# Optimization experiments

Hardware: AMD Instinct MI355X
Metric: run time of the kernel (lower is better)

## Reference

```python
import jax, jax.numpy as jnp
import numpy as np

DIM_MODEL = 512
INV_SCALE = DIM_MODEL ** (-0.5)  # NOTE: source DIVIDES by this, i.e. multiplies scores by sqrt(d)


def setup_inputs() -> dict:
    key = jax.random.key(0)
    ks = jax.random.split(key, 9)
    B, LQ, LKV, D = 32, 64, 4096, DIM_MODEL
    lim = 1.0 / np.sqrt(D)  # torch Linear default init range
    return {
        "x1": jax.random.normal(ks[0], (B, LQ, D), dtype=jnp.float32),
        "x2": jax.random.normal(ks[1], (B, LKV, D), dtype=jnp.float32),
        "mask": jnp.zeros((B, LQ, LKV), dtype=bool),
        "wq": jax.random.uniform(ks[2], (D, D), jnp.float32, -lim, lim),
        "bq": jax.random.uniform(ks[3], (D,), jnp.float32, -lim, lim),
        "wk": jax.random.uniform(ks[4], (D, D), jnp.float32, -lim, lim),
        "bk": jax.random.uniform(ks[5], (D,), jnp.float32, -lim, lim),
        "wv": jax.random.uniform(ks[6], (D, D), jnp.float32, -lim, lim),
        "bv": jax.random.uniform(ks[7], (D,), jnp.float32, -lim, lim),
    }


def reference(x1, x2, mask, wq, bq, wk, bk, wv, bv):
    # torch.nn.Linear: y = x @ W^T + b
    q = jnp.einsum("bqd,ed->bqe", x1, wq) + bq          # [B, LQ, D]
    k = jnp.einsum("bkd,ed->bke", x2, wk) + bk          # [B, LKV, D]
    v = jnp.einsum("bkd,ed->bke", x2, wv) + bv          # [B, LKV, D]
    qk = jnp.einsum("bqd,bkd->bqk", q, k)               # [B, LQ, LKV]
    scaled_qk = qk / INV_SCALE                           # faithful: divide by d^-0.5
    p = jax.nn.softmax(scaled_qk, axis=-1)
    # dropout p=0.0 -> identity; mask is unused in the original forward
    return jnp.einsum("bqk,bkd->bqd", p, v)              # [B, LQ, D]
```

## Files before the change

### kernel.cpp

```cpp
#include <hip/hip_runtime.h>
#include <math.h>


#define LQ 64
#define LKV 4096
#define NB 32
#define DM 512
#define SCALE 22.627416997969522f
#define KEYS_TOTAL (NB * LKV)
#define NCHUNK 16
#define CHUNK 256
#define PBS 264

typedef __attribute__((ext_vector_type(8))) short bf16x8;
typedef __attribute__((ext_vector_type(4))) float f32x4;
typedef __attribute__((ext_vector_type(8))) unsigned short u16x8;
typedef __attribute__((ext_vector_type(4))) unsigned short u16x4;

__device__ __forceinline__ unsigned short f2bf(float f) {
    unsigned u = __float_as_uint(f);
    u += 0x7fffu + ((u >> 16) & 1u);
    return (unsigned short)(u >> 16);
}
__device__ __forceinline__ float bf2f(unsigned short s) {
    return __uint_as_float(((unsigned)s) << 16);
}
__device__ __forceinline__ void gld16(const void* g, void* l) {
    __builtin_amdgcn_global_load_lds(
        (const __attribute__((address_space(1))) unsigned int*)g,
        (__attribute__((address_space(3))) unsigned int*)l, 16, 0, 0);
}

__device__ __forceinline__ void split8_body(const float* __restrict__ src,
                                            unsigned short* __restrict__ hi,
                                            unsigned short* __restrict__ lo, int blk) {
    size_t idx = ((size_t)blk * 256 + threadIdx.x) * 8;
    float4 a = *(const float4*)(src + idx);
    float4 b = *(const float4*)(src + idx + 4);
    float ff[8] = {a.x, a.y, a.z, a.w, b.x, b.y, b.z, b.w};
    u16x8 h, l;
#pragma unroll
    for (int i = 0; i < 8; ++i) {
        h[i] = f2bf(ff[i]);
        l[i] = f2bf(ff[i] - bf2f(h[i]));
    }
    *(u16x8*)(hi + idx) = h;
    *(u16x8*)(lo + idx) = l;
}

__global__ __launch_bounds__(256) void prep_kernel(
        const float* __restrict__ x1, const float* __restrict__ wq,
        const float* __restrict__ wk, const float* __restrict__ wv,
        unsigned short* __restrict__ x1h, unsigned short* __restrict__ x1l,
        unsigned short* __restrict__ wqh, unsigned short* __restrict__ wql,
        unsigned short* __restrict__ wkth, unsigned short* __restrict__ wktl,
        unsigned short* __restrict__ wvh, unsigned short* __restrict__ wvl) {
    __shared__ float T[64 * 65];
    int bid = blockIdx.x;
    if (bid < 512) { split8_body(x1, x1h, x1l, bid); return; }
    bid -= 512;
    if (bid < 128) { split8_body(wq, wqh, wql, bid); return; }
    bid -= 128;
    if (bid < 64) {
        const int bx = (bid & 7) * 64, by = (bid >> 3) * 64;
        const int t = threadIdx.x, col = t & 63, rg = t >> 6;
#pragma unroll
        for (int i = 0; i < 16; ++i) {
            int row = i * 4 + rg;
            T[col * 65 + row] = wk[(size_t)(by + row) * DM + bx + col];
        }
        __syncthreads();
#pragma unroll
        for (int i = 0; i < 16; ++i) {
            int row = i * 4 + rg;
            float v = T[row * 65 + col];
            unsigned short h = f2bf(v);
            wkth[(size_t)(bx + row) * DM + by + col] = h;
            wktl[(size_t)(bx + row) * DM + by + col] = f2bf(v - bf2f(h));
        }
        return;
    }
    bid -= 64;
    split8_body(wv, wvh, wvl, bid);
}

__global__ __launch_bounds__(256) void sgemm_kernel(
        const unsigned short* __restrict__ Ah_g, const unsigned short* __restrict__ Al_g,
        const unsigned short* __restrict__ Bh_g, const unsigned short* __restrict__ Bl_g,
        const float* __restrict__ bias, int mode,
        unsigned short* __restrict__ out0, unsigned short* __restrict__ out2l,
        float* __restrict__ outf) {
    __shared__ unsigned short smem[16384];
    unsigned short* Ah = smem;
    unsigned short* Al = smem + 4096;
    unsigned short* Bh = smem + 8192;
    unsigned short* Bl = smem + 12288;

    const int bn = blockIdx.x, bm = blockIdx.y;
    const int t = threadIdx.x, w = t >> 6, l = t & 63;
    const int wm = (w >> 1) * 64, wn = (w & 1) * 64;
    const int c16 = l & 15, q = l >> 4, q8 = q << 3;
    const int rB = l >> 2, cB = (l & 3) << 3;

    f32x4 acc[4][4];
#pragma unroll
    for (int i = 0; i < 4; ++i)
#pragma unroll
        for (int jj = 0; jj < 4; ++jj) acc[i][jj] = (f32x4){0.f,0.f,0.f,0.f};

    for (int k0 = 0; k0 < DM; k0 += 32) {
#pragma unroll
        for (int jj = 0; jj < 2; ++jj) {
            int r = w * 32 + jj * 16;
            size_t ga = (size_t)(bm * 128 + r + rB) * DM + k0 + cB;
            gld16(Ah_g + ga, &Ah[r * 32]);
            gld16(Al_g + ga, &Al[r * 32]);
            size_t gb = (size_t)(bn * 128 + r + rB) * DM + k0 + cB;
            gld16(Bh_g + gb, &Bh[r * 32]);
            gld16(Bl_g + gb, &Bl[r * 32]);
        }
        __syncthreads();
        bf16x8 ah[4], al[4];
#pragma unroll
        for (int mt = 0; mt < 4; ++mt) {
            ah[mt] = *(const bf16x8*)&Ah[(wm + mt*16 + c16) * 32 + q8];
            al[mt] = *(const bf16x8*)&Al[(wm + mt*16 + c16) * 32 + q8];
        }
#pragma unroll
        for (int nt = 0; nt < 4; ++nt) {
            bf16x8 bh = *(const bf16x8*)&Bh[(wn + nt*16 + c16) * 32 + q8];
            bf16x8 bl = *(const bf16x8*)&Bl[(wn + nt*16 + c16) * 32 + q8];
#pragma unroll
            for (int mt = 0; mt < 4; ++mt) {
                acc[mt][nt] = __builtin_amdgcn_mfma_f32_16x16x32_bf16(ah[mt], bh, acc[mt][nt], 0, 0, 0);
                acc[mt][nt] = __builtin_amdgcn_mfma_f32_16x16x32_bf16(al[mt], bh, acc[mt][nt], 0, 0, 0);
                acc[mt][nt] = __builtin_amdgcn_mfma_f32_16x16x32_bf16(ah[mt], bl, acc[mt][nt], 0, 0, 0);
            }
        }
        __syncthreads();
    }

#pragma unroll
    for (int mt = 0; mt < 4; ++mt)
#pragma unroll
        for (int nt = 0; nt < 4; ++nt) {
            int col = bn * 128 + wn + nt * 16 + c16;
            float bia = bias ? bias[col] : 0.f;
#pragma unroll
            for (int r = 0; r < 4; ++r) {
                size_t row = (size_t)bm * 128 + wm + mt * 16 + q * 4 + r;
                float y = acc[mt][nt][r] + bia;
                if (mode == 0) {
                    unsigned short h = f2bf(y);
                    out0[row * 1024 + col]       = h;
                    out0[row * 1024 + 512 + col] = f2bf(y - bf2f(h));
                } else if (mode == 1) {
                    outf[row * 512 + col] = y;
                } else {
                    unsigned short h = f2bf(y);
                    out0[row * 512 + col]  = h;
                    out2l[row * 512 + col] = f2bf(y - bf2f(h));
                }
            }
        }
}

__global__ __launch_bounds__(256) void prepVt_kernel(const float* __restrict__ src,
        unsigned short* __restrict__ x2ht) {
    __shared__ unsigned short T[128 * 136];
    const int d0 = blockIdx.x * 128, k0 = blockIdx.y * 128;
    const int t = threadIdx.x;
    const int cg = t & 31, rg = t >> 5;
#pragma unroll
    for (int i = 0; i < 16; ++i) {
        int row = i * 8 + rg;
        float4 v = *(const float4*)(src + (size_t)(k0 + row) * DM + d0 + cg * 4);
        float ff[4] = {v.x, v.y, v.z, v.w};
        int rsw = row ^ ((cg & 15) << 3);
#pragma unroll
        for (int j = 0; j < 4; ++j)
            T[(cg * 4 + j) * 136 + rsw] = f2bf(ff[j]);
    }
    __syncthreads();
#pragma unroll
    for (int ii = 0; ii < 8; ++ii) {
        int dl = ii * 16 + (t >> 4);
        int ko = (t & 15) * 8;
        u16x8 vv = *(const u16x8*)&T[dl * 136 + (ko ^ (((dl >> 2) & 15) << 3))];
        *(u16x8*)(x2ht + (size_t)(d0 + dl) * KEYS_TOTAL + k0 + ko) = vv;
    }
}

__global__ __launch_bounds__(512, 4) void attn_kernel(
        const unsigned short* __restrict__ Q2,
        const float* __restrict__ x2f,
        const unsigned short* __restrict__ Vt,
        float* __restrict__ Opart,
        float* __restrict__ ML) {
    __shared__ char smem_raw[81920];
    unsigned short* Pb = (unsigned short*)smem_raw;
    float* redb = (float*)(smem_raw + 66560);
    float* mrow = (float*)(smem_raw + 68608);
    float* lrow = (float*)(smem_raw + 68864);

    const int c = blockIdx.x, b = blockIdx.y;
    const int t = threadIdx.x, w = t >> 6, l = t & 63;
    const int c16 = l & 15, q = l >> 4, q8 = q << 3;
    const int rB = l >> 2, cB = (l & 3) << 3;
    const int rF = l >> 3, cF = (l & 7) << 2;
    const size_t key0 = (size_t)b * LKV + (size_t)c * CHUNK;

    f32x4 acc[4][2];
#pragma unroll
    for (int i = 0; i < 4; ++i)
#pragma unroll
        for (int jj = 0; jj < 2; ++jj) acc[i][jj] = (f32x4){0.f,0.f,0.f,0.f};

    auto stageQK = [&](int s, int k0) {
        char* base = smem_raw + s * 40960;
        unsigned short* Qh = (unsigned short*)base;
        unsigned short* Ql = (unsigned short*)(base + 4096);
        float* Kf = (float*)(base + 8192);
        if (w < 4)
            gld16(Q2 + (size_t)(b * 64 + w * 16 + rB) * 1024 + k0 + cB, &Qh[(w * 16) * 32]);
        else
            gld16(Q2 + (size_t)(b * 64 + (w - 4) * 16 + rB) * 1024 + 512 + k0 + cB, &Ql[((w - 4) * 16) * 32]);
#pragma unroll
        for (int i = 0; i < 4; ++i) {
            int r = w * 32 + i * 8;
            gld16(x2f + (key0 + r + rF) * DM + k0 + cF, &Kf[r * 32]);
        }
    };

    stageQK(0, 0);
    __syncthreads();
#pragma unroll 1
    for (int k0 = 0; k0 < DM; k0 += 32) {
        const int s = (k0 >> 5) & 1;
        if (k0 + 32 < DM) stageQK(s ^ 1, k0 + 32);
        const unsigned short* Qh = (const unsigned short*)(smem_raw + s * 40960);
        const unsigned short* Ql = Qh + 2048;
        const float* Kf = (const float*)(smem_raw + s * 40960 + 8192);
        bf16x8 ah[4], al[4];
#pragma unroll
        for (int mt = 0; mt < 4; ++mt) {
            ah[mt] = *(const bf16x8*)&Qh[(mt * 16 + c16) * 32 + q8];
            al[mt] = *(const bf16x8*)&Ql[(mt * 16 + c16) * 32 + q8];
        }
#pragma unroll
        for (int nt = 0; nt < 2; ++nt) {
            const float* kp = &Kf[(w * 32 + nt * 16 + c16) * 32 + q8];
            float4 f0 = *(const float4*)kp;
            float4 f1 = *(const float4*)(kp + 4);
            float ff[8] = {f0.x, f0.y, f0.z, f0.w, f1.x, f1.y, f1.z, f1.w};
            bf16x8 bh, bl;
#pragma unroll
            for (int i2 = 0; i2 < 8; ++i2) {
                unsigned short hb = f2bf(ff[i2]);
                bh[i2] = (short)hb;
                bl[i2] = (short)f2bf(ff[i2] - bf2f(hb));
            }
#pragma unroll
            for (int mt = 0; mt < 4; ++mt) {
                acc[mt][nt] = __builtin_amdgcn_mfma_f32_16x16x32_bf16(ah[mt], bh, acc[mt][nt], 0, 0, 0);
                acc[mt][nt] = __builtin_amdgcn_mfma_f32_16x16x32_bf16(al[mt], bh, acc[mt][nt], 0, 0, 0);
                acc[mt][nt] = __builtin_amdgcn_mfma_f32_16x16x32_bf16(ah[mt], bl, acc[mt][nt], 0, 0, 0);
            }
        }
        __syncthreads();
    }

    auto stagePV = [&](int s, int h, int ks) {
        unsigned short* Vb = (unsigned short*)(smem_raw + 33792 + s * 16384);
#pragma unroll
        for (int jj = 0; jj < 2; ++jj) {
            int dloc = w * 32 + jj * 16;
            gld16(Vt + (size_t)(h * 256 + dloc + rB) * KEYS_TOTAL + key0 + ks * 32 + cB,
                  &Vb[dloc * 32]);
        }
    };
    stagePV(0, 0, 0);

#pragma unroll
    for (int mt = 0; mt < 4; ++mt)
#pragma unroll
        for (int nt = 0; nt < 2; ++nt)
#pragma unroll
            for (int r = 0; r < 4; ++r) acc[mt][nt][r] *= SCALE;

    float rmax_[4][4];
#pragma unroll
    for (int mt = 0; mt < 4; ++mt)
#pragma unroll
        for (int r = 0; r < 4; ++r)
            rmax_[mt][r] = fmaxf(acc[mt][0][r], acc[mt][1][r]);
#pragma unroll
    for (int off = 1; off < 16; off <<= 1)
#pragma unroll
        for (int mt = 0; mt < 4; ++mt)
#pragma unroll
            for (int r = 0; r < 4; ++r)
                rmax_[mt][r] = fmaxf(rmax_[mt][r], __shfl_xor(rmax_[mt][r], off));
    if (c16 == 0) {
#pragma unroll
        for (int mt = 0; mt < 4; ++mt)
#pragma unroll
            for (int r = 0; r < 4; ++r) redb[w * 64 + mt * 16 + q * 4 + r] = rmax_[mt][r];
    }
    __syncthreads();
    if (t < 64) {
        float m = redb[t];
#pragma unroll
        for (int ww = 1; ww < 8; ++ww) m = fmaxf(m, redb[ww * 64 + t]);
        mrow[t] = m;
    }
    __syncthreads();

    float rsum_[4][4];
#pragma unroll
    for (int mt = 0; mt < 4; ++mt)
#pragma unroll
        for (int r = 0; r < 4; ++r) {
            float m = mrow[mt * 16 + q * 4 + r];
            float s = 0.f;
#pragma unroll
            for (int nt = 0; nt < 2; ++nt) {
                float e = __expf(acc[mt][nt][r] - m);
                acc[mt][nt][r] = e;
                s += e;
            }
            rsum_[mt][r] = s;
        }
#pragma unroll
    for (int off = 1; off < 16; off <<= 1)
#pragma unroll
        for (int mt = 0; mt < 4; ++mt)
#pragma unroll
            for (int r = 0; r < 4; ++r) rsum_[mt][r] += __shfl_xor(rsum_[mt][r], off);
    if (c16 == 0) {
#pragma unroll
        for (int mt = 0; mt < 4; ++mt)
#pragma unroll
            for (int r = 0; r < 4; ++r) redb[w * 64 + mt * 16 + q * 4 + r] = rsum_[mt][r];
    }
    __syncthreads();
    if (t < 64) {
        float s = redb[t];
#pragma unroll
        for (int ww = 1; ww < 8; ++ww) s += redb[ww * 64 + t];
        lrow[t] = s;
    }
#pragma unroll
    for (int mt = 0; mt < 4; ++mt)
#pragma unroll
        for (int nt = 0; nt < 2; ++nt)
#pragma unroll
            for (int r = 0; r < 4; ++r)
                Pb[(mt * 16 + q * 4 + r) * PBS + w * 32 + nt * 16 + c16] = f2bf(acc[mt][nt][r]);
    __syncthreads();

    f32x4 accO[4][4];
#pragma unroll
    for (int i = 0; i < 4; ++i)
#pragma unroll
        for (int jj = 0; jj < 4; ++jj) accO[i][jj] = (f32x4){0.f,0.f,0.f,0.f};

#pragma unroll 1
    for (int ks = 0; ks < 8; ++ks) {
        const int s = ks & 1;
        if (ks < 7) stagePV(s ^ 1, 0, ks + 1);
        else        stagePV(s ^ 1, 1, 0);
        const unsigned short* Vb = (const unsigned short*)(smem_raw + 33792 + s * 16384);
        bf16x8 ap[4];
#pragma unroll
        for (int mt = 0; mt < 4; ++mt)
            ap[mt] = *(const bf16x8*)&Pb[(mt * 16 + c16) * PBS + ks * 32 + q8];
#pragma unroll
        for (int nt = 0; nt < 2; ++nt) {
            bf16x8 bvv = *(const bf16x8*)&Vb[(w * 32 + nt * 16 + c16) * 32 + q8];
#pragma unroll
            for (int mt = 0; mt < 4; ++mt)
                accO[mt][nt] = __builtin_amdgcn_mfma_f32_16x16x32_bf16(ap[mt], bvv, accO[mt][nt], 0, 0, 0);
        }
        __syncthreads();
    }
#pragma unroll 1
    for (int ks = 0; ks < 8; ++ks) {
        const int s = ks & 1;
        if (ks < 7) stagePV(s ^ 1, 1, ks + 1);
        const unsigned short* Vb = (const unsigned short*)(smem_raw + 33792 + s * 16384);
        bf16x8 ap[4];
#pragma unroll
        for (int mt = 0; mt < 4; ++mt)
            ap[mt] = *(const bf16x8*)&Pb[(mt * 16 + c16) * PBS + ks * 32 + q8];
#pragma unroll
        for (int nt = 0; nt < 2; ++nt) {
            bf16x8 bvv = *(const bf16x8*)&Vb[(w * 32 + nt * 16 + c16) * 32 + q8];
#pragma unroll
            for (int mt = 0; mt < 4; ++mt)
                accO[mt][2 + nt] = __builtin_amdgcn_mfma_f32_16x16x32_bf16(ap[mt], bvv, accO[mt][2 + nt], 0, 0, 0);
        }
        __syncthreads();
    }

    const size_t part = (size_t)b * NCHUNK + c;
#pragma unroll
    for (int mt = 0; mt < 4; ++mt)
#pragma unroll
        for (int h = 0; h < 2; ++h)
#pragma unroll
            for (int nt = 0; nt < 2; ++nt) {
                int col = h * 256 + w * 32 + nt * 16 + c16;
#pragma unroll
                for (int r = 0; r < 4; ++r)
                    Opart[(part * 64 + mt * 16 + q * 4 + r) * 512 + col] = accO[mt][h * 2 + nt][r];
            }
    if (t < 64) {
        ML[part * 128 + t]      = mrow[t];
        ML[part * 128 + 64 + t] = lrow[t];
    }
}

__global__ __launch_bounds__(128) void combine_kernel(const float* __restrict__ Opart,
                                                      const float* __restrict__ ML,
                                                      unsigned short* __restrict__ Uh,
                                                      unsigned short* __restrict__ Ul) {
    const int b = blockIdx.x >> 6, row = blockIdx.x & 63;
    const int t = threadIdx.x;
    float m[NCHUNK], lv[NCHUNK];
    float M = -1e30f;
#pragma unroll
    for (int c = 0; c < NCHUNK; ++c) {
        m[c]  = ML[(size_t)(b * NCHUNK + c) * 128 + row];
        lv[c] = ML[(size_t)(b * NCHUNK + c) * 128 + 64 + row];
        M = fmaxf(M, m[c]);
    }
    float den = 0.f, wgt[NCHUNK];
#pragma unroll
    for (int c = 0; c < NCHUNK; ++c) { wgt[c] = __expf(m[c] - M); den += wgt[c] * lv[c]; }
    float4 o = make_float4(0.f, 0.f, 0.f, 0.f);
#pragma unroll
    for (int c = 0; c < NCHUNK; ++c) {
        float4 v = *(const float4*)&Opart[((size_t)(b * NCHUNK + c) * 64 + row) * 512 + t * 4];
        o.x += wgt[c] * v.x; o.y += wgt[c] * v.y; o.z += wgt[c] * v.z; o.w += wgt[c] * v.w;
    }
    const float inv = 1.f / den;
    float rr[4] = {o.x * inv, o.y * inv, o.z * inv, o.w * inv};
    u16x4 h, lo_;
#pragma unroll
    for (int j = 0; j < 4; ++j) {
        h[j]   = f2bf(rr[j]);
        lo_[j] = f2bf(rr[j] - bf2f(h[j]));
    }
    size_t base = ((size_t)(b * 64 + row)) * 512 + t * 4;
    *(u16x4*)&Uh[base] = h;
    *(u16x4*)&Ul[base] = lo_;
}

extern "C" void kernel_launch(void* const* d_in, const int* in_sizes, int n_in,
                              void* d_out, int out_size, void* d_ws, size_t ws_size,
                              hipStream_t stream) {
    const float* x1 = (const float*)d_in[0];
    const float* x2 = (const float*)d_in[1];
    const float* wq = (const float*)d_in[3];
    const float* bq = (const float*)d_in[4];
    const float* wk = (const float*)d_in[5];
    const float* wv = (const float*)d_in[7];
    const float* bv = (const float*)d_in[8];
    float* out = (float*)d_out;

    char* ws = (char*)d_ws;
    unsigned short* x2ht  = (unsigned short*)(ws);
    float*          Opart = (float*)(ws + 134217728);
    float*          ML    = (float*)(ws + 201326592);
    unsigned short* M2    = (unsigned short*)(ws + 201588736);
    unsigned short* x1h   = (unsigned short*)(ws + 205783040);
    unsigned short* x1l   = (unsigned short*)(ws + 207880192);
    unsigned short* Uh    = (unsigned short*)(ws + 209977344);
    unsigned short* Ul    = (unsigned short*)(ws + 212074496);
    unsigned short* q1h   = (unsigned short*)(ws + 214171648);
    unsigned short* q1l   = (unsigned short*)(ws + 216268800);
    unsigned short* wqh   = (unsigned short*)(ws + 218365952);
    unsigned short* wql   = (unsigned short*)(ws + 218890240);
    unsigned short* wkth  = (unsigned short*)(ws + 219414528);
    unsigned short* wktl  = (unsigned short*)(ws + 219938816);
    unsigned short* wvh   = (unsigned short*)(ws + 220463104);
    unsigned short* wvl   = (unsigned short*)(ws + 220987392);

    prepVt_kernel<<<dim3(4, 1024), 256, 0, stream>>>(x2, x2ht);

    prep_kernel<<<832, 256, 0, stream>>>(x1, wq, wk, wv,
                                         x1h, x1l, wqh, wql,
                                         wkth, wktl, wvh, wvl);

    sgemm_kernel<<<dim3(4, 16), 256, 0, stream>>>(x1h, x1l, wqh, wql,
                                                  bq, 2, q1h, q1l, nullptr);
    sgemm_kernel<<<dim3(4, 16), 256, 0, stream>>>(q1h, q1l, wkth, wktl,
                                                  nullptr, 0, M2, nullptr, nullptr);

    attn_kernel<<<dim3(NCHUNK, NB), 512, 0, stream>>>(M2, x2, x2ht, Opart, ML);
    combine_kernel<<<NB * LQ, 128, 0, stream>>>(Opart, ML, Uh, Ul);

    sgemm_kernel<<<dim3(4, 16), 256, 0, stream>>>(Uh, Ul, wvh, wvl,
                                                  bv, 1, nullptr, nullptr, out);
}
```

Before: 596.3 us.

## Deepen async LDS prefetch with explicit vmcnt waits, raw barriers and setprio

Replaces __syncthreads-based double buffering with a two-stage-ahead prefetch scheme. Both buffers are preloaded, each iteration waits on a partial vmcnt before a raw s_barrier, and the next-next tile is issued after compute, so global-to-LDS loads stay in flight across iterations. MFMA sections are wrapped in s_setprio to favour math waves, and reduction barriers use lgkmcnt waits instead of the full sync. This relies on hand-counted vmcnt values matching the number of outstanding loads per stage. A wrong count would cause races.

```diff
diff --git a/kernel.cpp b/kernel.cpp
--- a/kernel.cpp
+++ b/kernel.cpp
@@ -231,13 +231,24 @@
             gld16(x2f + (key0 + r + rF) * DM + k0 + cF, &Kf[r * 32]);
         }
     };
+    auto stagePV = [&](int s, int h, int ks) {
+        unsigned short* Vb = (unsigned short*)(smem_raw + 33792 + s * 16384);
+#pragma unroll
+        for (int jj = 0; jj < 2; ++jj) {
+            int dloc = w * 32 + jj * 16;
+            gld16(Vt + (size_t)(h * 256 + dloc + rB) * KEYS_TOTAL + key0 + ks * 32 + cB,
+                  &Vb[dloc * 32]);
+        }
+    };
 
     stageQK(0, 0);
-    __syncthreads();
+    stageQK(1, 32);
 #pragma unroll 1
     for (int k0 = 0; k0 < DM; k0 += 32) {
         const int s = (k0 >> 5) & 1;
-        if (k0 + 32 < DM) stageQK(s ^ 1, k0 + 32);
+        if (k0 + 32 < DM) asm volatile("s_waitcnt vmcnt(5)" ::: "memory");
+        else              asm volatile("s_waitcnt vmcnt(0)" ::: "memory");
+        __builtin_amdgcn_s_barrier();
         const unsigned short* Qh = (const unsigned short*)(smem_raw + s * 40960);
         const unsigned short* Ql = Qh + 2048;
         const float* Kf = (const float*)(smem_raw + s * 40960 + 8192);
@@ -247,6 +258,7 @@
             ah[mt] = *(const bf16x8*)&Qh[(mt * 16 + c16) * 32 + q8];
             al[mt] = *(const bf16x8*)&Ql[(mt * 16 + c16) * 32 + q8];
         }
+        __builtin_amdgcn_s_setprio(1);
 #pragma unroll
         for (int nt = 0; nt < 2; ++nt) {
             const float* kp = &Kf[(w * 32 + nt * 16 + c16) * 32 + q8];
@@ -267,19 +279,13 @@
                 acc[mt][nt] = __builtin_amdgcn_mfma_f32_16x16x32_bf16(ah[mt], bl, acc[mt][nt], 0, 0, 0);
             }
         }
-        __syncthreads();
-    }
-
-    auto stagePV = [&](int s, int h, int ks) {
-        unsigned short* Vb = (unsigned short*)(smem_raw + 33792 + s * 16384);
-#pragma unroll
-        for (int jj = 0; jj < 2; ++jj) {
-            int dloc = w * 32 + jj * 16;
-            gld16(Vt + (size_t)(h * 256 + dloc + rB) * KEYS_TOTAL + key0 + ks * 32 + cB,
-                  &Vb[dloc * 32]);
-        }
-    };
+        __builtin_amdgcn_s_setprio(0);
+        __builtin_amdgcn_s_barrier();
+        if (k0 + 64 < DM) stageQK(s, k0 + 64);
+    }
+
     stagePV(0, 0, 0);
+    stagePV(1, 0, 1);
 
 #pragma unroll
     for (int mt = 0; mt < 4; ++mt)
@@ -307,14 +313,16 @@
 #pragma unroll
             for (int r = 0; r < 4; ++r) redb[w * 64 + mt * 16 + q * 4 + r] = rmax_[mt][r];
     }
-    __syncthreads();
+    asm volatile("s_waitcnt lgkmcnt(0)" ::: "memory");
+    __builtin_amdgcn_s_barrier();
     if (t < 64) {
         float m = redb[t];
 #pragma unroll
         for (int ww = 1; ww < 8; ++ww) m = fmaxf(m, redb[ww * 64 + t]);
         mrow[t] = m;
     }
-    __syncthreads();
+    asm volatile("s_waitcnt lgkmcnt(0)" ::: "memory");
+    __builtin_amdgcn_s_barrier();
 
     float rsum_[4][4];
 #pragma unroll
@@ -343,7 +351,8 @@
 #pragma unroll
             for (int r = 0; r < 4; ++r) redb[w * 64 + mt * 16 + q * 4 + r] = rsum_[mt][r];
     }
-    __syncthreads();
+    asm volatile("s_waitcnt lgkmcnt(0)" ::: "memory");
+    __builtin_amdgcn_s_barrier();
     if (t < 64) {
         float s = redb[t];
 #pragma unroll
@@ -357,7 +366,8 @@
 #pragma unroll
             for (int r = 0; r < 4; ++r)
                 Pb[(mt * 16 + q * 4 + r) * PBS + w * 32 + nt * 16 + c16] = f2bf(acc[mt][nt][r]);
-    __syncthreads();
+    asm volatile("s_waitcnt lgkmcnt(0)" ::: "memory");
+    __builtin_amdgcn_s_barrier();
 
     f32x4 accO[4][4];
 #pragma unroll
@@ -368,13 +378,14 @@
 #pragma unroll 1
     for (int ks = 0; ks < 8; ++ks) {
         const int s = ks & 1;
-        if (ks < 7) stagePV(s ^ 1, 0, ks + 1);
-        else        stagePV(s ^ 1, 1, 0);
+        asm volatile("s_waitcnt vmcnt(2)" ::: "memory");
+        __builtin_amdgcn_s_barrier();
         const unsigned short* Vb = (const unsigned short*)(smem_raw + 33792 + s * 16384);
         bf16x8 ap[4];
 #pragma unroll
         for (int mt = 0; mt < 4; ++mt)
             ap[mt] = *(const bf16x8*)&Pb[(mt * 16 + c16) * PBS + ks * 32 + q8];
+        __builtin_amdgcn_s_setprio(1);
 #pragma unroll
         for (int nt = 0; nt < 2; ++nt) {
             bf16x8 bvv = *(const bf16x8*)&Vb[(w * 32 + nt * 16 + c16) * 32 + q8];
@@ -382,17 +393,24 @@
             for (int mt = 0; mt < 4; ++mt)
                 accO[mt][nt] = __builtin_amdgcn_mfma_f32_16x16x32_bf16(ap[mt], bvv, accO[mt][nt], 0, 0, 0);
         }
-        __syncthreads();
+        __builtin_amdgcn_s_setprio(0);
+        __builtin_amdgcn_s_barrier();
+        if (ks < 6)       stagePV(s, 0, ks + 2);
+        else if (ks == 6) stagePV(0, 1, 0);
+        else              stagePV(1, 1, 1);
     }
 #pragma unroll 1
     for (int ks = 0; ks < 8; ++ks) {
         const int s = ks & 1;
-        if (ks < 7) stagePV(s ^ 1, 1, ks + 1);
+        if (ks < 7) asm volatile("s_waitcnt vmcnt(2)" ::: "memory");
+        else        asm volatile("s_waitcnt vmcnt(0)" ::: "memory");
+        __builtin_amdgcn_s_barrier();
         const unsigned short* Vb = (const unsigned short*)(smem_raw + 33792 + s * 16384);
         bf16x8 ap[4];
 #pragma unroll
         for (int mt = 0; mt < 4; ++mt)
             ap[mt] = *(const bf16x8*)&Pb[(mt * 16 + c16) * PBS + ks * 32 + q8];
+        __builtin_amdgcn_s_setprio(1);
 #pragma unroll
         for (int nt = 0; nt < 2; ++nt) {
             bf16x8 bvv = *(const bf16x8*)&Vb[(w * 32 + nt * 16 + c16) * 32 + q8];
@@ -400,7 +418,9 @@
             for (int mt = 0; mt < 4; ++mt)
                 accO[mt][2 + nt] = __builtin_amdgcn_mfma_f32_16x16x32_bf16(ap[mt], bvv, accO[mt][2 + nt], 0, 0, 0);
         }
-        __syncthreads();
+        __builtin_amdgcn_s_setprio(0);
+        __builtin_amdgcn_s_barrier();
+        if (ks < 6) stagePV(s, 1, ks + 2);
     }
 
     const size_t part = (size_t)b * NCHUNK + c;
```

After: 598.0 us. Within noise of the previous version (+0.3%).
